# Kernel optimization log

Hardware: AMD Instinct MI355X
Metric: run time of the kernel (lower is better)

Reference implementation:

```python
import jax, jax.numpy as jnp
import numpy as np

B, S, D = 4, 2048, 2048
H = 16
Q_LORA = 1536
KV_LORA = 512
D_NOPE = 128
D_ROPE = 64
D_V = 128
MLP = 8192
EPS = 1e-6
THETA = 10000.0


def rmsnorm(x, scale, eps=EPS):
    var = jnp.mean(jnp.square(x.astype(jnp.float32)), axis=-1, keepdims=True)
    return (x * jax.lax.rsqrt(var + eps)).astype(x.dtype) * scale


def rope(x, positions):
    # x: [B, S, H, d], positions: [B, S]
    d = x.shape[-1]
    inv_freq = 1.0 / (THETA ** (jnp.arange(0, d, 2, dtype=jnp.float32) / d))
    ang = positions.astype(jnp.float32)[..., None] * inv_freq  # [B,S,d/2]
    cos = jnp.cos(ang)[:, :, None, :]
    sin = jnp.sin(ang)[:, :, None, :]
    x1, x2 = jnp.split(x, 2, axis=-1)
    return jnp.concatenate([x1 * cos - x2 * sin, x2 * cos + x1 * sin], axis=-1)


def setup_inputs() -> dict:
    key = jax.random.key(0)
    ks = jax.random.split(key, 16)
    sd = lambda fan: 1.0 / np.sqrt(fan)
    inp = {
        'inputs': jax.random.normal(ks[0], (B, S, D), jnp.float32),
        'decoder_segment_ids': jnp.ones((B, S), jnp.int32),
        'decoder_positions': jnp.broadcast_to(jnp.arange(S, dtype=jnp.int32), (B, S)),
        'pre_ln_scale': jnp.ones((D,), jnp.float32),
        'post_ln_scale': jnp.ones((D,), jnp.float32),
        'q_ln_scale': jnp.ones((Q_LORA,), jnp.float32),
        'kv_ln_scale': jnp.ones((KV_LORA,), jnp.float32),
        'wq_a': jax.random.normal(ks[1], (D, Q_LORA), jnp.float32) * sd(D),
        'wq_b': jax.random.normal(ks[2], (Q_LORA, H, D_NOPE + D_ROPE), jnp.float32) * sd(Q_LORA),
        'wkv_a': jax.random.normal(ks[3], (D, KV_LORA + D_ROPE), jnp.float32) * sd(D),
        'wkv_b': jax.random.normal(ks[4], (KV_LORA, H, D_NOPE + D_V), jnp.float32) * sd(KV_LORA),
        'wo_attn': jax.random.normal(ks[5], (H, D_V, D), jnp.float32) * sd(H * D_V),
        'wi_0': jax.random.normal(ks[6], (D, MLP), jnp.float32) * sd(D),
        'wi_1': jax.random.normal(ks[7], (D, MLP), jnp.float32) * sd(D),
        'wo_mlp': jax.random.normal(ks[8], (MLP, D), jnp.float32) * sd(MLP),
    }
    return inp


def reference(inputs, decoder_segment_ids, decoder_positions, pre_ln_scale, post_ln_scale,
              q_ln_scale, kv_ln_scale, wq_a, wq_b, wkv_a, wkv_b, wo_attn, wi_0, wi_1, wo_mlp):
    # ---- pre-norm ----
    lnx = rmsnorm(inputs, pre_ln_scale)

    # ---- MLA attention ----
    # low-rank query: down-proj, norm, up-proj
    q_c = rmsnorm(lnx @ wq_a, q_ln_scale)                       # [B,S,Q_LORA]
    q = jnp.einsum('bsr,rhd->bshd', q_c, wq_b)                  # [B,S,H,nope+rope]
    q_nope, q_rope = q[..., :D_NOPE], q[..., D_NOPE:]

    # compressed kv + decoupled rope key
    kv = lnx @ wkv_a                                            # [B,S,KV_LORA+rope]
    c_kv = rmsnorm(kv[..., :KV_LORA], kv_ln_scale)
    k_rope = kv[..., KV_LORA:][:, :, None, :]                   # [B,S,1,rope]
    kvu = jnp.einsum('bsr,rhd->bshd', c_kv, wkv_b)              # [B,S,H,nope+v]
    k_nope, v = kvu[..., :D_NOPE], kvu[..., D_NOPE:]

    q_rope = rope(q_rope, decoder_positions)
    k_rope = rope(k_rope, decoder_positions)
    k_rope = jnp.broadcast_to(k_rope, (B, S, H, D_ROPE))

    qf = jnp.concatenate([q_nope, q_rope], axis=-1)             # [B,S,H,192]
    kf = jnp.concatenate([k_nope, k_rope], axis=-1)

    scale = 1.0 / np.sqrt(D_NOPE + D_ROPE)
    scores = jnp.einsum('bqhd,bkhd->bhqk', qf, kf) * scale      # [B,H,S,S]

    pos = decoder_positions
    seg = decoder_segment_ids
    mask = (pos[:, :, None] >= pos[:, None, :]) & (seg[:, :, None] == seg[:, None, :])
    scores = jnp.where(mask[:, None, :, :], scores, -1e9)
    probs = jax.nn.softmax(scores, axis=-1)

    attn = jnp.einsum('bhqk,bkhd->bqhd', probs, v)              # [B,S,H,D_V]
    attn_out = jnp.einsum('bqhd,hdm->bqm', attn, wo_attn)       # [B,S,D]

    # ---- residual + post-norm ----
    intermediate = inputs + attn_out
    hidden = rmsnorm(intermediate, post_ln_scale)

    # ---- gated MLP (silu * linear) ----
    mlp = (jax.nn.silu(hidden @ wi_0) * (hidden @ wi_1)) @ wo_mlp

    return mlp + intermediate
```

## Files before the change

### kernel.cpp

```cpp
#include <hip/hip_runtime.h>
#include <stdint.h>

typedef unsigned short u16;
typedef __bf16 bf16x8 __attribute__((ext_vector_type(8)));
typedef float f32x4 __attribute__((ext_vector_type(4)));

#define B_ 4
#define S_ 2048
#define H_ 16
#define TOK (B_*S_)
#define MFMA_B16 __builtin_amdgcn_mfma_f32_16x16x32_bf16

__device__ __forceinline__ u16 f32_bf16(float f) {
    union { float f; unsigned int u; } x; x.f = f;
    return (u16)((x.u + 0x7fffu + ((x.u >> 16) & 1u)) >> 16);
}
__device__ __forceinline__ float bf2f(u16 v) {
    union { unsigned int u; float f; } x; x.u = ((unsigned int)v) << 16; return x.f;
}
__device__ __forceinline__ void gld_lds16(const u16* g, u16* lds) {
    __builtin_amdgcn_global_load_lds(
        (const __attribute__((address_space(1))) unsigned int*)g,
        (__attribute__((address_space(3))) unsigned int*)lds, 16, 0, 0);
}

__global__ void fill_sentinel(float* o, int n) {
    int i = blockIdx.x * 256 + threadIdx.x;
    if (i < n) o[i] = 12345.0f;
}

__global__ __launch_bounds__(256) void transpose_f32_bf16(const float* __restrict__ in, u16* __restrict__ out,
                                                          int K, int N, int Npad) {
    __shared__ float t[32][33];
    int nb = blockIdx.x * 32, kb = blockIdx.y * 32;
    int c = threadIdx.x & 31, r = threadIdx.x >> 5;
#pragma unroll
    for (int i = 0; i < 4; ++i) {
        int kk = kb + r + i * 8, nn = nb + c;
        t[r + i * 8][c] = (kk < K && nn < N) ? in[(size_t)kk * N + nn] : 0.f;
    }
    __syncthreads();
#pragma unroll
    for (int i = 0; i < 4; ++i) {
        int no = nb + r + i * 8, ko = kb + c;
        if (no < Npad && ko < K) out[(size_t)no * K + ko] = f32_bf16(t[c][r + i * 8]);
    }
}

__global__ __launch_bounds__(256) void rmsnorm_f32(const float* __restrict__ in, const float* __restrict__ sc,
                                                   u16* __restrict__ out, int N) {
    int row = blockIdx.x;
    const float* x = in + (size_t)row * N;
    float ss = 0.f;
    for (int c = threadIdx.x * 4; c < N; c += 1024) {
        float4 v = *(const float4*)(x + c);
        ss += v.x * v.x + v.y * v.y + v.z * v.z + v.w * v.w;
    }
#pragma unroll
    for (int off = 32; off; off >>= 1) ss += __shfl_down(ss, off);
    __shared__ float red[4];
    if ((threadIdx.x & 63) == 0) red[threadIdx.x >> 6] = ss;
    __syncthreads();
    float rs = rsqrtf((red[0] + red[1] + red[2] + red[3]) / (float)N + 1e-6f);
    for (int c = threadIdx.x * 4; c < N; c += 1024) {
        float4 v = *(const float4*)(x + c);
        float4 s4 = *(const float4*)(sc + c);
        ushort4 ov;
        ov.x = f32_bf16(v.x * rs * s4.x);
        ov.y = f32_bf16(v.y * rs * s4.y);
        ov.z = f32_bf16(v.z * rs * s4.z);
        ov.w = f32_bf16(v.w * rs * s4.w);
        *(ushort4*)&out[(size_t)row * N + c] = ov;
    }
}

__global__ __launch_bounds__(256) void rmsnorm_bf16(const u16* __restrict__ in, const float* __restrict__ sc,
                                                    u16* __restrict__ out, int N) {
    int row = blockIdx.x;
    const u16* x = in + (size_t)row * N;
    float ss = 0.f;
    for (int c = threadIdx.x * 8; c < N; c += 2048) {
        ushort4 v0 = *(const ushort4*)(x + c);
        ushort4 v1 = *(const ushort4*)(x + c + 4);
        float f0 = bf2f(v0.x), f1 = bf2f(v0.y), f2 = bf2f(v0.z), f3 = bf2f(v0.w);
        float f4 = bf2f(v1.x), f5 = bf2f(v1.y), f6 = bf2f(v1.z), f7 = bf2f(v1.w);
        ss += f0*f0 + f1*f1 + f2*f2 + f3*f3 + f4*f4 + f5*f5 + f6*f6 + f7*f7;
    }
#pragma unroll
    for (int off = 32; off; off >>= 1) ss += __shfl_down(ss, off);
    __shared__ float red[4];
    if ((threadIdx.x & 63) == 0) red[threadIdx.x >> 6] = ss;
    __syncthreads();
    float rs = rsqrtf((red[0] + red[1] + red[2] + red[3]) / (float)N + 1e-6f);
    for (int c = threadIdx.x * 8; c < N; c += 2048) {
        ushort4 v0 = *(const ushort4*)(x + c);
        ushort4 v1 = *(const ushort4*)(x + c + 4);
        ushort4 o0, o1;
        o0.x = f32_bf16(bf2f(v0.x) * rs * sc[c + 0]);
        o0.y = f32_bf16(bf2f(v0.y) * rs * sc[c + 1]);
        o0.z = f32_bf16(bf2f(v0.z) * rs * sc[c + 2]);
        o0.w = f32_bf16(bf2f(v0.w) * rs * sc[c + 3]);
        o1.x = f32_bf16(bf2f(v1.x) * rs * sc[c + 4]);
        o1.y = f32_bf16(bf2f(v1.y) * rs * sc[c + 5]);
        o1.z = f32_bf16(bf2f(v1.z) * rs * sc[c + 6]);
        o1.w = f32_bf16(bf2f(v1.w) * rs * sc[c + 7]);
        *(ushort4*)&out[(size_t)row * N + c] = o0;
        *(ushort4*)&out[(size_t)row * N + c + 4] = o1;
    }
}

__global__ __launch_bounds__(128) void kv_post(const u16* __restrict__ kv, const float* __restrict__ scale,
                                               const int* __restrict__ pos, u16* __restrict__ ckv,
                                               u16* __restrict__ kr) {
    int row = blockIdx.x;
    const u16* x = kv + (size_t)row * 640;
    int c = threadIdx.x * 4;
    ushort4 v = *(const ushort4*)(x + c);
    float f0 = bf2f(v.x), f1 = bf2f(v.y), f2 = bf2f(v.z), f3 = bf2f(v.w);
    float ss = f0*f0 + f1*f1 + f2*f2 + f3*f3;
#pragma unroll
    for (int off = 32; off; off >>= 1) ss += __shfl_down(ss, off);
    __shared__ float red[2];
    if ((threadIdx.x & 63) == 0) red[threadIdx.x >> 6] = ss;
    __syncthreads();
    float rs = rsqrtf((red[0] + red[1]) * (1.f / 512.f) + 1e-6f);
    float4 s4 = *(const float4*)(scale + c);
    ushort4 ov;
    ov.x = f32_bf16(f0 * rs * s4.x);
    ov.y = f32_bf16(f1 * rs * s4.y);
    ov.z = f32_bf16(f2 * rs * s4.z);
    ov.w = f32_bf16(f3 * rs * s4.w);
    *(ushort4*)&ckv[(size_t)row * 512 + c] = ov;
    if (threadIdx.x < 32) {
        int i = threadIdx.x;
        float x1 = bf2f(x[512 + i]), x2 = bf2f(x[544 + i]);
        float inv = expf(-(float)(2 * i) * (1.f / 64.f) * 9.2103403719761836f);
        float ang = (float)pos[row] * inv;
        float sn, cs; sincosf(ang, &sn, &cs);
        kr[(size_t)row * 64 + i]      = f32_bf16(x1 * cs - x2 * sn);
        kr[(size_t)row * 64 + 32 + i] = f32_bf16(x2 * cs + x1 * sn);
    }
}

__global__ __launch_bounds__(64) void q_rope_inplace(u16* __restrict__ q, const int* __restrict__ pos) {
    int token = blockIdx.x, h = blockIdx.y;
    u16* p = q + ((size_t)token * 16 + h) * 192;
    int t = threadIdx.x, i = t & 31;
    float x1 = bf2f(p[128 + i]), x2 = bf2f(p[160 + i]);
    float inv = expf(-(float)(2 * i) * (1.f / 64.f) * 9.2103403719761836f);
    float ang = (float)pos[token] * inv;
    float sn, cs; sincosf(ang, &sn, &cs);
    float val = (t < 32) ? (x1 * cs - x2 * sn) : (x2 * cs + x1 * sn);
    p[128 + t] = f32_bf16(val);
}

__global__ __launch_bounds__(320) void kv_build(const u16* __restrict__ kvu, const u16* __restrict__ kr,
                                                u16* __restrict__ kf, u16* __restrict__ vf, int tok0) {
    int local = blockIdx.x, h = blockIdx.y;
    int token = tok0 + local;
    int b = token >> 11, s = token & 2047;
    int bh = b * 16 + h;
    int tile = s >> 6, ki = s & 63;
    const u16* u = kvu + ((size_t)local * 16 + h) * 256;
    int t = threadIdx.x;
    if (t < 192) {
        u16 val = (t < 128) ? u[t] : kr[(size_t)token * 64 + (t - 128)];
        int byte = (ki * 384 + t * 2) ^ ((ki & 7) << 4);
        kf[(size_t)bh * (S_ * 192) + (size_t)tile * 12288 + (byte >> 1)] = val;
    } else {
        int dv = t - 192;
        u16 val = u[128 + dv];
        int byte = (dv * 128 + ki * 2) ^ ((dv & 7) << 4);
        vf[(size_t)bh * (S_ * 128) + (size_t)tile * 8192 + (byte >> 1)] = val;
    }
}

__global__ __launch_bounds__(256) void gemm128(const u16* __restrict__ A, const u16* __restrict__ Bt,
                                               u16* __restrict__ C, int M, int N, int K) {
    __shared__ u16 As[128 * 32];
    __shared__ u16 Bs[128 * 32];
    const int l = threadIdx.x & 63, w = threadIdx.x >> 6;
    const int wr = w >> 1, wc = w & 1;
    const int m0 = blockIdx.y * 128, n0 = blockIdx.x * 128;
    const int lm = l & 15, lg = l >> 4;
    const int srow = l >> 2, sk = (l & 3) * 8;
    f32x4 acc[4][4] = {};
    for (int k0 = 0; k0 < K; k0 += 32) {
#pragma unroll
        for (int i = 0; i < 2; ++i) {
            int c = w * 2 + i;
            gld_lds16(A  + (size_t)(m0 + c * 16 + srow) * K + k0 + sk, &As[c * 512]);
            gld_lds16(Bt + (size_t)(n0 + c * 16 + srow) * K + k0 + sk, &Bs[c * 512]);
        }
        __syncthreads();
        bf16x8 a[4], b[4];
#pragma unroll
        for (int m = 0; m < 4; ++m) a[m] = *(const bf16x8*)&As[(wr * 64 + m * 16 + lm) * 32 + lg * 8];
#pragma unroll
        for (int n = 0; n < 4; ++n) b[n] = *(const bf16x8*)&Bs[(wc * 64 + n * 16 + lm) * 32 + lg * 8];
#pragma unroll
        for (int m = 0; m < 4; ++m)
#pragma unroll
            for (int n = 0; n < 4; ++n)
                acc[m][n] = MFMA_B16(a[m], b[n], acc[m][n], 0, 0, 0);
        __syncthreads();
    }
#pragma unroll
    for (int m = 0; m < 4; ++m)
#pragma unroll
        for (int j = 0; j < 4; ++j) {
            int row = m0 + wr * 64 + m * 16 + lg * 4 + j;
            size_t base = (size_t)row * N + n0 + wc * 64;
#pragma unroll
            for (int n = 0; n < 4; ++n)
                C[base + n * 16 + lm] = f32_bf16(acc[m][n][j]);
        }
}

template<int EPI>
__global__ __launch_bounds__(512, 2) void gemm256(const u16* __restrict__ A, const u16* __restrict__ Bt,
                                                  void* __restrict__ Cv, const void* __restrict__ Rv,
                                                  int M, int N, int K) {
    __shared__ u16 lds[65536];
    char* ldsb = (char*)lds;
    const int tid = threadIdx.x;
    const int l = tid & 63, w = tid >> 6;
    const int wr = w >> 2, wcn = w & 3;
    const int lm = l & 15, lg = l >> 4;
    const int m0 = blockIdx.y * 256, n0 = blockIdx.x * 256;

    int gm[2], gk[2];
#pragma unroll
    for (int ld = 0; ld < 2; ++ld) {
        int P = tid * 16 + ld * 8192;
        int row = P >> 7;
        int un = (P & 127) ^ ((row & 7) << 4);
        gm[ld] = row * 2 + (un >> 6);
        gk[ld] = (un & 63) >> 1;
    }
    const u16* Ab = A + (size_t)m0 * K;
    const u16* Bb = Bt + (size_t)n0 * K;

    f32x4 acc[8][4] = {};

    auto stageA = [&](int t) {
#pragma unroll
        for (int ld = 0; ld < 2; ++ld)
            gld_lds16(Ab + (size_t)gm[ld] * K + t * 32 + gk[ld],
                      (u16*)(ldsb + (t & 3) * 32768 + tid * 16 + ld * 8192));
    };
    auto stageB = [&](int t) {
#pragma unroll
        for (int ld = 0; ld < 2; ++ld)
            gld_lds16(Bb + (size_t)gm[ld] * K + t * 32 + gk[ld],
                      (u16*)(ldsb + (t & 3) * 32768 + 16384 + tid * 16 + ld * 8192));
    };
    auto readA = [&](int buf, int fm) -> bf16x8 {
        int m = wr * 128 + fm * 16 + lm;
        int off = ((m & 1) * 64 + lg * 16) ^ (((m >> 1) & 7) << 4);
        return *(const bf16x8*)(ldsb + buf * 32768 + (m >> 1) * 128 + off);
    };
    auto readB = [&](int buf, int fn) -> bf16x8 {
        int n = wcn * 64 + fn * 16 + lm;
        int off = ((n & 1) * 64 + lg * 16) ^ (((n >> 1) & 7) << 4);
        return *(const bf16x8*)(ldsb + buf * 32768 + 16384 + (n >> 1) * 128 + off);
    };

    const int ntile = K >> 5;
    stageA(0); stageB(0);
    stageA(1); stageB(1);
    stageA(2); stageB(2);

#pragma unroll 1
    for (int t = 0; t < ntile; ++t) {
        const int buf = t & 3;
        if (t + 2 < ntile)      { asm volatile("s_waitcnt vmcnt(8)" ::: "memory"); }
        else if (t + 1 < ntile) { asm volatile("s_waitcnt vmcnt(4)" ::: "memory"); }
        else                    { asm volatile("s_waitcnt vmcnt(0)" ::: "memory"); }
        __builtin_amdgcn_s_barrier();
        __builtin_amdgcn_sched_barrier(0);
        if (t + 3 < ntile) { stageA(t + 3); stageB(t + 3); }
        bf16x8 b0 = readB(buf, 0), b1 = readB(buf, 1), b2 = readB(buf, 2), b3 = readB(buf, 3);
        bf16x8 a0 = readA(buf, 0), a1 = readA(buf, 1), a2 = readA(buf, 2), a3 = readA(buf, 3);
        bf16x8 a4 = readA(buf, 4), a5 = readA(buf, 5), a6 = readA(buf, 6), a7 = readA(buf, 7);
        acc[0][0] = MFMA_B16(a0, b0, acc[0][0], 0, 0, 0);
        acc[0][1] = MFMA_B16(a0, b1, acc[0][1], 0, 0, 0);
        acc[0][2] = MFMA_B16(a0, b2, acc[0][2], 0, 0, 0);
        acc[0][3] = MFMA_B16(a0, b3, acc[0][3], 0, 0, 0);
        acc[1][0] = MFMA_B16(a1, b0, acc[1][0], 0, 0, 0);
        acc[1][1] = MFMA_B16(a1, b1, acc[1][1], 0, 0, 0);
        acc[1][2] = MFMA_B16(a1, b2, acc[1][2], 0, 0, 0);
        acc[1][3] = MFMA_B16(a1, b3, acc[1][3], 0, 0, 0);
        acc[2][0] = MFMA_B16(a2, b0, acc[2][0], 0, 0, 0);
        acc[2][1] = MFMA_B16(a2, b1, acc[2][1], 0, 0, 0);
        acc[2][2] = MFMA_B16(a2, b2, acc[2][2], 0, 0, 0);
        acc[2][3] = MFMA_B16(a2, b3, acc[2][3], 0, 0, 0);
        acc[3][0] = MFMA_B16(a3, b0, acc[3][0], 0, 0, 0);
        acc[3][1] = MFMA_B16(a3, b1, acc[3][1], 0, 0, 0);
        acc[3][2] = MFMA_B16(a3, b2, acc[3][2], 0, 0, 0);
        acc[3][3] = MFMA_B16(a3, b3, acc[3][3], 0, 0, 0);
        acc[4][0] = MFMA_B16(a4, b0, acc[4][0], 0, 0, 0);
        acc[4][1] = MFMA_B16(a4, b1, acc[4][1], 0, 0, 0);
        acc[4][2] = MFMA_B16(a4, b2, acc[4][2], 0, 0, 0);
        acc[4][3] = MFMA_B16(a4, b3, acc[4][3], 0, 0, 0);
        acc[5][0] = MFMA_B16(a5, b0, acc[5][0], 0, 0, 0);
        acc[5][1] = MFMA_B16(a5, b1, acc[5][1], 0, 0, 0);
        acc[5][2] = MFMA_B16(a5, b2, acc[5][2], 0, 0, 0);
        acc[5][3] = MFMA_B16(a5, b3, acc[5][3], 0, 0, 0);
        acc[6][0] = MFMA_B16(a6, b0, acc[6][0], 0, 0, 0);
        acc[6][1] = MFMA_B16(a6, b1, acc[6][1], 0, 0, 0);
        acc[6][2] = MFMA_B16(a6, b2, acc[6][2], 0, 0, 0);
        acc[6][3] = MFMA_B16(a6, b3, acc[6][3], 0, 0, 0);
        acc[7][0] = MFMA_B16(a7, b0, acc[7][0], 0, 0, 0);
        acc[7][1] = MFMA_B16(a7, b1, acc[7][1], 0, 0, 0);
        acc[7][2] = MFMA_B16(a7, b2, acc[7][2], 0, 0, 0);
        acc[7][3] = MFMA_B16(a7, b3, acc[7][3], 0, 0, 0);
    }
#pragma unroll
    for (int fm = 0; fm < 8; ++fm)
#pragma unroll
        for (int j = 0; j < 4; ++j) {
            int row = m0 + wr * 128 + fm * 16 + lg * 4 + j;
            size_t base = (size_t)row * N + n0 + wcn * 64;
#pragma unroll
            for (int fn = 0; fn < 4; ++fn) {
                size_t idx = base + fn * 16 + lm;
                float v = acc[fm][fn][j];
                if (EPI == 0) {
                    ((u16*)Cv)[idx] = f32_bf16(v);
                } else if (EPI == 1) {
                    ((float*)Cv)[idx] = v + ((const float*)Rv)[idx];
                } else {
                    float x0 = bf2f(((const u16*)Rv)[idx]);
                    float sl = x0 / (1.f + expf(-x0));
                    ((u16*)Cv)[idx] = f32_bf16(sl * v);
                }
            }
        }
}

__global__ __launch_bounds__(256) void attn_fwd(const u16* __restrict__ qf, const u16* __restrict__ kfs,
                                                const u16* __restrict__ vfs, u16* __restrict__ attn) {
    __shared__ u16 Ks[2][64 * 192];
    __shared__ u16 Vs[2][128 * 64];
    __shared__ u16 Ps[4][1024];
    const int px = blockIdx.x;
    const int bh = blockIdx.y;
    const int b = bh >> 4, h = bh & 15;
    const int l = threadIdx.x & 63, w = threadIdx.x >> 6;
    const int lm = l & 15, g = l >> 4;
    const u16* kb0 = kfs + (size_t)bh * (S_ * 192);
    const u16* vb0 = vfs + (size_t)bh * (S_ * 128);
    const float scale = 0.07216878364870322f;

    auto stageKV = [&](int kt2, int d2) {
        const u16* kc = kb0 + (size_t)kt2 * 12288;
        const u16* vc = vb0 + (size_t)kt2 * 8192;
#pragma unroll
        for (int i = 0; i < 6; ++i) {
            int c = w + i * 4;
            gld_lds16(kc + c * 512 + l * 8, &Ks[d2][c * 512]);
        }
#pragma unroll
        for (int i = 0; i < 4; ++i) {
            int c = w + i * 4;
            gld_lds16(vc + c * 512 + l * 8, &Vs[d2][c * 512]);
        }
    };

    for (int pass = 0; pass < 2; ++pass) {
        const int qb = pass ? (31 - px) : px;
        const int qrow = qb * 64 + w * 16 + lm;
        const u16* qp = qf + (((size_t)(b * S_ + qrow)) * 16 + h) * 192 + g * 8;
        bf16x8 qr[6];
#pragma unroll
        for (int c = 0; c < 6; ++c) qr[c] = *(const bf16x8*)(qp + c * 32);
        f32x4 o[8] = {};
        float mrow[4] = {-1e30f, -1e30f, -1e30f, -1e30f};
        float lrow[4] = {0.f, 0.f, 0.f, 0.f};
        __syncthreads();
        stageKV(0, 0);
        for (int kt = 0; kt <= qb; ++kt) {
            const int d = kt & 1;
            __syncthreads();
            if (kt < qb) stageKV(kt + 1, d ^ 1);
            f32x4 sc[4] = {};
#pragma unroll
            for (int nf = 0; nf < 4; ++nf) {
                int key = nf * 16 + lm;
                int kswz = (key & 7) << 4;
#pragma unroll
                for (int c = 0; c < 6; ++c) {
                    int byte = (key * 384 + (c * 32 + g * 8) * 2) ^ kswz;
                    bf16x8 kv = *(const bf16x8*)((const char*)&Ks[d][0] + byte);
                    sc[nf] = MFMA_B16(qr[c], kv, sc[nf], 0, 0, 0);
                }
            }
#pragma unroll
            for (int j = 0; j < 4; ++j) {
                const int q_g = qb * 64 + w * 16 + g * 4 + j;
                float mx = -1e30f;
#pragma unroll
                for (int nf = 0; nf < 4; ++nf) {
                    int key_g = kt * 64 + nf * 16 + lm;
                    float v = sc[nf][j] * scale;
                    v = (key_g > q_g) ? -1e30f : v;
                    sc[nf][j] = v;
                    mx = fmaxf(mx, v);
                }
                mx = fmaxf(mx, __shfl_xor(mx, 1));
                mx = fmaxf(mx, __shfl_xor(mx, 2));
                mx = fmaxf(mx, __shfl_xor(mx, 4));
                mx = fmaxf(mx, __shfl_xor(mx, 8));
                float newm = fmaxf(mrow[j], mx);
                float fac = __expf(mrow[j] - newm);
                mrow[j] = newm;
                float rs = 0.f;
                u16 pb[4];
#pragma unroll
                for (int nf = 0; nf < 4; ++nf) {
                    float pv = __expf(sc[nf][j] - newm);
                    rs += pv;
                    pb[nf] = f32_bf16(pv);
                }
                rs += __shfl_xor(rs, 1);
                rs += __shfl_xor(rs, 2);
                rs += __shfl_xor(rs, 4);
                rs += __shfl_xor(rs, 8);
                lrow[j] = lrow[j] * fac + rs;
#pragma unroll
                for (int n = 0; n < 8; ++n) o[n][j] *= fac;
                int row = g * 4 + j;
                int rswz = (row & 7) << 4;
#pragma unroll
                for (int nf = 0; nf < 4; ++nf) {
                    int byte = (row * 128 + (nf * 16 + lm) * 2) ^ rswz;
                    *(u16*)((char*)&Ps[w][0] + byte) = pb[nf];
                }
            }
#pragma unroll
            for (int kc2 = 0; kc2 < 2; ++kc2) {
                int pbyte = (lm * 128 + (kc2 * 32 + g * 8) * 2) ^ ((lm & 7) << 4);
                bf16x8 pa = *(const bf16x8*)((const char*)&Ps[w][0] + pbyte);
#pragma unroll
                for (int n = 0; n < 8; ++n) {
                    int dv = n * 16 + lm;
                    int vbyte = (dv * 128 + (kc2 * 32 + g * 8) * 2) ^ ((dv & 7) << 4);
                    bf16x8 vv = *(const bf16x8*)((const char*)&Vs[d][0] + vbyte);
                    o[n] = MFMA_B16(pa, vv, o[n], 0, 0, 0);
                }
            }
        }
#pragma unroll
        for (int j = 0; j < 4; ++j) {
            float inv = 1.f / lrow[j];
            int s = qb * 64 + w * 16 + g * 4 + j;
            size_t base = ((size_t)(b * S_ + s)) * (H_ * 128) + h * 128;
#pragma unroll
            for (int n = 0; n < 8; ++n)
                attn[base + n * 16 + lm] = f32_bf16(o[n][j] * inv);
        }
    }
}

extern "C" void kernel_launch(void* const* d_in, const int* in_sizes, int n_in,
                              void* d_out, int out_size, void* d_ws, size_t ws_size,
                              hipStream_t stream) {
    (void)in_sizes; (void)n_in;
    const float* inputs = (const float*)d_in[0];
    const int*   pos    = (const int*)d_in[2];
    const float* pre_s  = (const float*)d_in[3];
    const float* post_s = (const float*)d_in[4];
    const float* q_s    = (const float*)d_in[5];
    const float* kv_s   = (const float*)d_in[6];
    const float* wq_a   = (const float*)d_in[7];
    const float* wq_b   = (const float*)d_in[8];
    const float* wkv_a  = (const float*)d_in[9];
    const float* wkv_b  = (const float*)d_in[10];
    const float* wo_at  = (const float*)d_in[11];
    const float* wi0    = (const float*)d_in[12];
    const float* wi1    = (const float*)d_in[13];
    const float* wom    = (const float*)d_in[14];
    float* out = (float*)d_out;

    char* p = (char*)d_ws;
    auto alloc = [&](size_t n) { char* r = p; p += (n + 255) & ~(size_t)255; return r; };
    char* R1   = alloc((size_t)134217728);
    u16* vf    = (u16*)alloc((size_t)33554432);
    u16* aslot = (u16*)alloc((size_t)33554432);
    u16* wslot = (u16*)alloc((size_t)33554432);
    u16* ckv   = (u16*)alloc((size_t)8388608);
    u16* krope = (u16*)alloc((size_t)1048576);
    if ((size_t)(p - (char*)d_ws) > ws_size) {
        fill_sentinel<<<(out_size + 255) / 256, 256, 0, stream>>>(out, out_size);
        return;
    }
    u16* kf    = (u16*)R1;
    u16* q_c   = (u16*)R1;
    u16* kvtmp = (u16*)(R1 + 25165824);
    u16* q     = (u16*)(R1 + 50331648);
    u16* lnx   = (u16*)(R1 + 100663296);
    u16* kvu   = (u16*)(R1 + 100663296);
    u16* X     = (u16*)R1;

    rmsnorm_f32<<<TOK, 256, 0, stream>>>(inputs, pre_s, lnx, 2048);
    transpose_f32_bf16<<<dim3(48, 64), 256, 0, stream>>>(wq_a, wslot, 2048, 1536, 1536);
    gemm256<0><<<dim3(6, 32), 512, 0, stream>>>(lnx, wslot, q_c, nullptr, TOK, 1536, 2048);
    rmsnorm_bf16<<<TOK, 256, 0, stream>>>(q_c, q_s, q_c, 1536);
    transpose_f32_bf16<<<dim3(20, 64), 256, 0, stream>>>(wkv_a, wslot, 2048, 576, 640);
    gemm128<<<dim3(5, 64), 256, 0, stream>>>(lnx, wslot, kvtmp, TOK, 640, 2048);
    kv_post<<<TOK, 128, 0, stream>>>(kvtmp, kv_s, pos, ckv, krope);
    transpose_f32_bf16<<<dim3(96, 48), 256, 0, stream>>>(wq_b, wslot, 1536, 3072, 3072);
    gemm256<0><<<dim3(12, 32), 512, 0, stream>>>(q_c, wslot, q, nullptr, TOK, 3072, 1536);
    q_rope_inplace<<<dim3(TOK, 16), 64, 0, stream>>>(q, pos);
    transpose_f32_bf16<<<dim3(128, 16), 256, 0, stream>>>(wkv_b, wslot, 512, 4096, 4096);
    for (int ch = 0; ch < 2; ++ch) {
        int t0 = ch * 4096;
        gemm256<0><<<dim3(16, 16), 512, 0, stream>>>(ckv + (size_t)t0 * 512, wslot, kvu, nullptr, 4096, 4096, 512);
        kv_build<<<dim3(4096, 16), 320, 0, stream>>>(kvu, krope, kf, vf, t0);
    }
    attn_fwd<<<dim3(16, 64), 256, 0, stream>>>(q, kf, vf, aslot);
    transpose_f32_bf16<<<dim3(64, 64), 256, 0, stream>>>(wo_at, wslot, 2048, 2048, 2048);
    gemm256<1><<<dim3(8, 32), 512, 0, stream>>>(aslot, wslot, out, inputs, TOK, 2048, 2048);
    rmsnorm_f32<<<TOK, 256, 0, stream>>>(out, post_s, aslot, 2048);
    transpose_f32_bf16<<<dim3(256, 64), 256, 0, stream>>>(wi0, wslot, 2048, 8192, 8192);
    gemm256<0><<<dim3(32, 32), 512, 0, stream>>>(aslot, wslot, X, nullptr, TOK, 8192, 2048);
    transpose_f32_bf16<<<dim3(256, 64), 256, 0, stream>>>(wi1, wslot, 2048, 8192, 8192);
    gemm256<2><<<dim3(32, 32), 512, 0, stream>>>(aslot, wslot, X, X, TOK, 8192, 2048);
    transpose_f32_bf16<<<dim3(64, 256), 256, 0, stream>>>(wom, wslot, 8192, 2048, 2048);
    gemm256<1><<<dim3(8, 32), 512, 0, stream>>>(X, wslot, out, out, TOK, 2048, 8192);
}
```

Before: 1.801 ms.

## Shrink LDS buffering in GEMM and attention to raise occupancy, remap attention blocks

```diff
diff --git a/kernel.cpp b/kernel.cpp
--- a/kernel.cpp
+++ b/kernel.cpp
@@ -10,6 +10,8 @@
 #define H_ 16
 #define TOK (B_*S_)
 #define MFMA_B16 __builtin_amdgcn_mfma_f32_16x16x32_bf16
+#define LGKM0 asm volatile("s_waitcnt lgkmcnt(0)" ::: "memory")
+#define VMC(n) asm volatile("s_waitcnt vmcnt(" #n ")" ::: "memory")
 
 __device__ __forceinline__ u16 f32_bf16(float f) {
     union { float f; unsigned int u; } x; x.f = f;
@@ -218,10 +220,10 @@
 }
 
 template<int EPI>
-__global__ __launch_bounds__(512, 2) void gemm256(const u16* __restrict__ A, const u16* __restrict__ Bt,
+__global__ __launch_bounds__(512, 4) void gemm256(const u16* __restrict__ A, const u16* __restrict__ Bt,
                                                   void* __restrict__ Cv, const void* __restrict__ Rv,
                                                   int M, int N, int K) {
-    __shared__ u16 lds[65536];
+    __shared__ u16 lds[32768];
     char* ldsb = (char*)lds;
     const int tid = threadIdx.x;
     const int l = tid & 63, w = tid >> 6;
@@ -247,13 +249,13 @@
 #pragma unroll
         for (int ld = 0; ld < 2; ++ld)
             gld_lds16(Ab + (size_t)gm[ld] * K + t * 32 + gk[ld],
-                      (u16*)(ldsb + (t & 3) * 32768 + tid * 16 + ld * 8192));
+                      (u16*)(ldsb + (t & 1) * 32768 + tid * 16 + ld * 8192));
     };
     auto stageB = [&](int t) {
 #pragma unroll
         for (int ld = 0; ld < 2; ++ld)
             gld_lds16(Bb + (size_t)gm[ld] * K + t * 32 + gk[ld],
-                      (u16*)(ldsb + (t & 3) * 32768 + 16384 + tid * 16 + ld * 8192));
+                      (u16*)(ldsb + (t & 1) * 32768 + 16384 + tid * 16 + ld * 8192));
     };
     auto readA = [&](int buf, int fm) -> bf16x8 {
         int m = wr * 128 + fm * 16 + lm;
@@ -268,18 +270,14 @@
 
     const int ntile = K >> 5;
     stageA(0); stageB(0);
-    stageA(1); stageB(1);
-    stageA(2); stageB(2);
 
 #pragma unroll 1
     for (int t = 0; t < ntile; ++t) {
-        const int buf = t & 3;
-        if (t + 2 < ntile)      { asm volatile("s_waitcnt vmcnt(8)" ::: "memory"); }
-        else if (t + 1 < ntile) { asm volatile("s_waitcnt vmcnt(4)" ::: "memory"); }
-        else                    { asm volatile("s_waitcnt vmcnt(0)" ::: "memory"); }
+        const int buf = t & 1;
+        VMC(0);
         __builtin_amdgcn_s_barrier();
         __builtin_amdgcn_sched_barrier(0);
-        if (t + 3 < ntile) { stageA(t + 3); stageB(t + 3); }
+        if (t + 1 < ntile) { stageA(t + 1); stageB(t + 1); }
         bf16x8 b0 = readB(buf, 0), b1 = readB(buf, 1), b2 = readB(buf, 2), b3 = readB(buf, 3);
         bf16x8 a0 = readA(buf, 0), a1 = readA(buf, 1), a2 = readA(buf, 2), a3 = readA(buf, 3);
         bf16x8 a4 = readA(buf, 4), a5 = readA(buf, 5), a6 = readA(buf, 6), a7 = readA(buf, 7);
@@ -339,13 +337,15 @@
         }
 }
 
-__global__ __launch_bounds__(256) void attn_fwd(const u16* __restrict__ qf, const u16* __restrict__ kfs,
-                                                const u16* __restrict__ vfs, u16* __restrict__ attn) {
-    __shared__ u16 Ks[2][64 * 192];
-    __shared__ u16 Vs[2][128 * 64];
+__global__ __launch_bounds__(256, 3) void attn_fwd(const u16* __restrict__ qf, const u16* __restrict__ kfs,
+                                                   const u16* __restrict__ vfs, u16* __restrict__ attn) {
+    __shared__ u16 Ks[64 * 192];
+    __shared__ u16 Vs[128 * 64];
     __shared__ u16 Ps[4][1024];
-    const int px = blockIdx.x;
-    const int bh = blockIdx.y;
+    const int lin = blockIdx.y * gridDim.x + blockIdx.x;
+    const int xcd = lin & 7, j = lin >> 3;
+    const int bh = xcd * 8 + (j >> 4);
+    const int px = j & 15;
     const int b = bh >> 4, h = bh & 15;
     const int l = threadIdx.x & 63, w = threadIdx.x >> 6;
     const int lm = l & 15, g = l >> 4;
@@ -353,20 +353,24 @@
     const u16* vb0 = vfs + (size_t)bh * (S_ * 128);
     const float scale = 0.07216878364870322f;
 
-    auto stageKV = [&](int kt2, int d2) {
+    auto stageK = [&](int kt2) {
         const u16* kc = kb0 + (size_t)kt2 * 12288;
-        const u16* vc = vb0 + (size_t)kt2 * 8192;
 #pragma unroll
         for (int i = 0; i < 6; ++i) {
             int c = w + i * 4;
-            gld_lds16(kc + c * 512 + l * 8, &Ks[d2][c * 512]);
-        }
+            gld_lds16(kc + c * 512 + l * 8, &Ks[c * 512]);
+        }
+    };
+    auto stageV = [&](int kt2) {
+        const u16* vc = vb0 + (size_t)kt2 * 8192;
 #pragma unroll
         for (int i = 0; i < 4; ++i) {
             int c = w + i * 4;
-            gld_lds16(vc + c * 512 + l * 8, &Vs[d2][c * 512]);
+            gld_lds16(vc + c * 512 + l * 8, &Vs[c * 512]);
         }
     };
+
+    stageK(0);
 
     for (int pass = 0; pass < 2; ++pass) {
         const int qb = pass ? (31 - px) : px;
@@ -378,12 +382,9 @@
         f32x4 o[8] = {};
         float mrow[4] = {-1e30f, -1e30f, -1e30f, -1e30f};
         float lrow[4] = {0.f, 0.f, 0.f, 0.f};
-        __syncthreads();
-        stageKV(0, 0);
         for (int kt = 0; kt <= qb; ++kt) {
-            const int d = kt & 1;
             __syncthreads();
-            if (kt < qb) stageKV(kt + 1, d ^ 1);
+            stageV(kt);
             f32x4 sc[4] = {};
 #pragma unroll
             for (int nf = 0; nf < 4; ++nf) {
@@ -392,34 +393,37 @@
 #pragma unroll
                 for (int c = 0; c < 6; ++c) {
                     int byte = (key * 384 + (c * 32 + g * 8) * 2) ^ kswz;
-                    bf16x8 kv = *(const bf16x8*)((const char*)&Ks[d][0] + byte);
+                    bf16x8 kv = *(const bf16x8*)((const char*)Ks + byte);
                     sc[nf] = MFMA_B16(qr[c], kv, sc[nf], 0, 0, 0);
                 }
             }
-#pragma unroll
-            for (int j = 0; j < 4; ++j) {
-                const int q_g = qb * 64 + w * 16 + g * 4 + j;
+            LGKM0;
+            __builtin_amdgcn_s_barrier();
+            if (kt < qb) stageK(kt + 1);
+#pragma unroll
+            for (int jj = 0; jj < 4; ++jj) {
+                const int q_g = qb * 64 + w * 16 + g * 4 + jj;
                 float mx = -1e30f;
 #pragma unroll
                 for (int nf = 0; nf < 4; ++nf) {
                     int key_g = kt * 64 + nf * 16 + lm;
-                    float v = sc[nf][j] * scale;
+                    float v = sc[nf][jj] * scale;
                     v = (key_g > q_g) ? -1e30f : v;
-                    sc[nf][j] = v;
+                    sc[nf][jj] = v;
                     mx = fmaxf(mx, v);
                 }
                 mx = fmaxf(mx, __shfl_xor(mx, 1));
                 mx = fmaxf(mx, __shfl_xor(mx, 2));
                 mx = fmaxf(mx, __shfl_xor(mx, 4));
                 mx = fmaxf(mx, __shfl_xor(mx, 8));
-                float newm = fmaxf(mrow[j], mx);
-                float fac = __expf(mrow[j] - newm);
-                mrow[j] = newm;
+                float newm = fmaxf(mrow[jj], mx);
+                float fac = __expf(mrow[jj] - newm);
+                mrow[jj] = newm;
                 float rs = 0.f;
                 u16 pb[4];
 #pragma unroll
                 for (int nf = 0; nf < 4; ++nf) {
-                    float pv = __expf(sc[nf][j] - newm);
+                    float pv = __expf(sc[nf][jj] - newm);
                     rs += pv;
                     pb[nf] = f32_bf16(pv);
                 }
@@ -427,10 +431,10 @@
                 rs += __shfl_xor(rs, 2);
                 rs += __shfl_xor(rs, 4);
                 rs += __shfl_xor(rs, 8);
-                lrow[j] = lrow[j] * fac + rs;
-#pragma unroll
-                for (int n = 0; n < 8; ++n) o[n][j] *= fac;
-                int row = g * 4 + j;
+                lrow[jj] = lrow[jj] * fac + rs;
+#pragma unroll
+                for (int n = 0; n < 8; ++n) o[n][jj] *= fac;
+                int row = g * 4 + jj;
                 int rswz = (row & 7) << 4;
 #pragma unroll
                 for (int nf = 0; nf < 4; ++nf) {
@@ -438,6 +442,9 @@
                     *(u16*)((char*)&Ps[w][0] + byte) = pb[nf];
                 }
             }
+            if (kt < qb) { VMC(6); } else { VMC(0); }
+            __builtin_amdgcn_s_barrier();
+            __builtin_amdgcn_sched_barrier(0);
 #pragma unroll
             for (int kc2 = 0; kc2 < 2; ++kc2) {
                 int pbyte = (lm * 128 + (kc2 * 32 + g * 8) * 2) ^ ((lm & 7) << 4);
@@ -446,20 +453,21 @@
                 for (int n = 0; n < 8; ++n) {
                     int dv = n * 16 + lm;
                     int vbyte = (dv * 128 + (kc2 * 32 + g * 8) * 2) ^ ((dv & 7) << 4);
-                    bf16x8 vv = *(const bf16x8*)((const char*)&Vs[d][0] + vbyte);
+                    bf16x8 vv = *(const bf16x8*)((const char*)Vs + vbyte);
                     o[n] = MFMA_B16(pa, vv, o[n], 0, 0, 0);
                 }
             }
         }
 #pragma unroll
-        for (int j = 0; j < 4; ++j) {
-            float inv = 1.f / lrow[j];
-            int s = qb * 64 + w * 16 + g * 4 + j;
+        for (int jj = 0; jj < 4; ++jj) {
+            float inv = 1.f / lrow[jj];
+            int s = qb * 64 + w * 16 + g * 4 + jj;
             size_t base = ((size_t)(b * S_ + s)) * (H_ * 128) + h * 128;
 #pragma unroll
             for (int n = 0; n < 8; ++n)
-                attn[base + n * 16 + lm] = f32_bf16(o[n][j] * inv);
-        }
+                attn[base + n * 16 + lm] = f32_bf16(o[n][jj] * inv);
+        }
+        if (pass == 0) stageK(0);
     }
 }
 
```

New measurement: 6.387 ms. +254.7%, slower.
